# Kernel tuning notes

Measured on AMD Instinct MI355X. Metric: run time of the kernel, lower is better.

Reference implementation:

```python
import jax, jax.numpy as jnp
import numpy as np

B, D, H, W, T, C = 2, 16, 16, 16, 16, 96
NH = 4                      # num_heads
WS = (4, 4, 4, 4)           # window size
SS = (2, 2, 2, 2)           # shift size
EPS = 1e-5
HIDDEN = 4 * C


def _compute_mask():
    # Standard Swin shifted-window attention mask, extended to 4D.
    img = np.zeros((D, H, W, T), np.float32)
    sl = [[slice(0, -WS[i]), slice(-WS[i], -SS[i]), slice(-SS[i], None)] for i in range(4)]
    cnt = 0
    for a in sl[0]:
        for b in sl[1]:
            for c in sl[2]:
                for d in sl[3]:
                    img[a, b, c, d] = cnt
                    cnt += 1
    x = img.reshape(D // WS[0], WS[0], H // WS[1], WS[1], W // WS[2], WS[2], T // WS[3], WS[3])
    x = x.transpose(0, 2, 4, 6, 1, 3, 5, 7).reshape(-1, WS[0] * WS[1] * WS[2] * WS[3])
    diff = x[:, None, :] - x[:, :, None]
    return np.where(diff != 0, np.float32(-100.0), np.float32(0.0))


def setup_inputs() -> dict:
    key = jax.random.key(0)
    ks = jax.random.split(key, 6)
    w = lambda k, shape: jax.random.normal(k, shape, jnp.float32) * 0.02
    return {
        'x': jax.random.normal(ks[0], (B, D, H, W, T, C), jnp.float32),
        'mask_matrix': jnp.asarray(_compute_mask()),
        'norm1_g': jnp.ones((C,), jnp.float32), 'norm1_b': jnp.zeros((C,), jnp.float32),
        'qkv_w': w(ks[1], (3 * C, C)), 'qkv_b': jnp.zeros((3 * C,), jnp.float32),
        'proj_w': w(ks[2], (C, C)), 'proj_b': jnp.zeros((C,), jnp.float32),
        'norm2_g': jnp.ones((C,), jnp.float32), 'norm2_b': jnp.zeros((C,), jnp.float32),
        'fc1_w': w(ks[3], (HIDDEN, C)), 'fc1_b': jnp.zeros((HIDDEN,), jnp.float32),
        'fc2_w': w(ks[4], (C, HIDDEN)), 'fc2_b': jnp.zeros((C,), jnp.float32),
    }


def _ln(x, g, b):
    mu = jnp.mean(x, -1, keepdims=True)
    var = jnp.var(x, -1, keepdims=True)
    return (x - mu) * jax.lax.rsqrt(var + EPS) * g + b


def _partition(x):
    # (B, D, H, W, T, C) -> (B*nw, N, C)
    b, c = x.shape[0], x.shape[-1]
    x = x.reshape(b, D // WS[0], WS[0], H // WS[1], WS[1], W // WS[2], WS[2], T // WS[3], WS[3], c)
    x = x.transpose(0, 1, 3, 5, 7, 2, 4, 6, 8, 9)
    return x.reshape(-1, WS[0] * WS[1] * WS[2] * WS[3], c)


def _reverse(win, b):
    c = win.shape[-1]
    x = win.reshape(b, D // WS[0], H // WS[1], W // WS[2], T // WS[3], WS[0], WS[1], WS[2], WS[3], c)
    x = x.transpose(0, 1, 5, 2, 6, 3, 7, 4, 8, 9)
    return x.reshape(b, D, H, W, T, c)


def reference(x, mask_matrix, norm1_g, norm1_b, qkv_w, qkv_b, proj_w, proj_b,
              norm2_g, norm2_b, fc1_w, fc1_b, fc2_w, fc2_b):
    b, c = x.shape[0], x.shape[-1]
    hd = c // NH
    scale = hd ** -0.5
    shortcut = x
    # norm -> (no pad needed: dims divisible by window) -> cyclic shift
    xn = _ln(x, norm1_g, norm1_b)
    xs = jnp.roll(xn, shift=(-SS[0], -SS[1], -SS[2], -SS[3]), axis=(1, 2, 3, 4))
    win = _partition(xs)                              # (B_, N, C)
    B_, N, _ = win.shape
    qkv = (win @ qkv_w.T + qkv_b).reshape(B_, N, 3, NH, hd).transpose(2, 0, 3, 1, 4)
    q, k, v = qkv[0] * scale, qkv[1], qkv[2]          # (B_, NH, N, hd)
    attn = jnp.einsum('bhid,bhjd->bhij', q, k)        # (B_, NH, N, N)
    nw = mask_matrix.shape[0]
    attn = attn.reshape(B_ // nw, nw, NH, N, N) + mask_matrix[None, :, None]
    attn = jax.nn.softmax(attn.reshape(B_, NH, N, N), axis=-1)
    out = jnp.einsum('bhij,bhjd->bhid', attn, v)
    out = out.transpose(0, 2, 1, 3).reshape(B_, N, c)
    out = out @ proj_w.T + proj_b
    xr = _reverse(out, b)
    xr = jnp.roll(xr, shift=SS, axis=(1, 2, 3, 4))    # reverse cyclic shift
    x = shortcut + xr
    # MLP block
    h = _ln(x, norm2_g, norm2_b)
    h = jax.nn.gelu(h @ fc1_w.T + fc1_b, approximate=False)
    return x + (h @ fc2_w.T + fc2_b)
```

## Files before the change

### kernel.cpp

```cpp
#include <hip/hip_runtime.h>

#define TOK   131072
#define BWIN  512

typedef __attribute__((ext_vector_type(8))) short bf16x8;
typedef __attribute__((ext_vector_type(4))) float f32x4;

__device__ __forceinline__ unsigned short f2us(float f) {
  union { float f; unsigned int i; } x; x.f = f;
  return (unsigned short)((x.i + 0x7fffu + ((x.i >> 16) & 1u)) >> 16);
}
__device__ __forceinline__ unsigned cvtpk(float lo, float hi) {
  unsigned r;
  asm("v_cvt_pk_bf16_f32 %0, %1, %2" : "=v"(r) : "v"(lo), "v"(hi));
  return r;
}
typedef const __attribute__((address_space(1))) unsigned int GU32;
typedef __attribute__((address_space(3))) unsigned int LU32;
__device__ __forceinline__ void gld16(const void* g, void* l) {
  __builtin_amdgcn_global_load_lds((GU32*)g, (LU32*)l, 16, 0, 0);
}

#define IW1   0
#define IW2   40960
#define IQKV  81920
#define IPROJ 116736
#define IMG_SHORTS 133120

__global__ __launch_bounds__(256) void k_prepw(
    const float* __restrict__ fc1_w, const float* __restrict__ fc2_w,
    const float* __restrict__ qkv_w, const float* __restrict__ proj_w,
    unsigned short* __restrict__ img) {
  int i = blockIdx.x * 256 + threadIdx.x;
  float v = 0.f;
  if (i < 40960) {
    int nc = i / 10240, k = i % 10240, r = k / 104, c = k % 104;
    if (k < 9984 && c < 96) v = fc1_w[(size_t)(nc * 96 + r) * 96 + c];
  } else if (i < 81920) {
    int j = i - 40960;
    int nc = j / 10240, k = j % 10240, r = k / 104, c = k % 104;
    if (k < 9984 && c < 96) v = fc2_w[(size_t)r * 384 + nc * 96 + c];
  } else if (i < 116736) {
    int j = i - 81920;
    int h = j / 8704, k = j % 8704, r = k / 104, c = k % 104;
    if (k < 8320 && r < 72 && c < 96) {
      int grp = r / 24, rr = r - grp * 24;
      v = qkv_w[(size_t)(grp * 96 + h * 24 + rr) * 96 + c];
    }
  } else {
    int j = i - 116736;
    int h = j / 4096, k = j % 4096, r = k / 40, c = k % 40;
    if (k < 3840 && c < 24) v = proj_w[(size_t)r * 96 + h * 24 + c];
  }
  img[i] = f2us(v);
}

__global__ __launch_bounds__(256) void k_ln1(const float* __restrict__ x,
                                             const float* __restrict__ g,
                                             const float* __restrict__ b,
                                             unsigned short* __restrict__ xn) {
  const int wave = threadIdx.x >> 6, lane = threadIdx.x & 63;
  const int t = blockIdx.x * 4 + wave;
  const int b_ = t >> 8, n = t & 255;
  const int batch = b_ >> 8, wi = b_ & 255;
  const int wd = (wi >> 6) & 3, wh = (wi >> 4) & 3, ww = (wi >> 2) & 3, wt = wi & 3;
  const int aa = (n >> 6) & 3, bb = (n >> 4) & 3, cc = (n >> 2) & 3, dd = n & 3;
  const int sd = (wd * 4 + aa + 2) & 15, sh = (wh * 4 + bb + 2) & 15;
  const int sw = (ww * 4 + cc + 2) & 15, st = (wt * 4 + dd + 2) & 15;
  const size_t gg = ((((size_t)(batch * 16 + sd) * 16 + sh) * 16 + sw) * 16 + st);

  float2 f;
  if (lane < 48) f = *(const float2*)(x + gg * 96 + 2 * lane);
  else { f.x = 0.f; f.y = 0.f; }
  float s = f.x + f.y, q2 = f.x * f.x + f.y * f.y;
  #pragma unroll
  for (int m = 1; m < 64; m <<= 1) { s += __shfl_xor(s, m, 64); q2 += __shfl_xor(q2, m, 64); }
  const float mu = s * (1.f / 96.f);
  const float var = q2 * (1.f / 96.f) - mu * mu;
  const float rs = rsqrtf(fmaxf(var, 0.f) + 1e-5f);
  if (lane < 48) {
    float a0 = (f.x - mu) * rs * g[2 * lane]     + b[2 * lane];
    float a1 = (f.y - mu) * rs * g[2 * lane + 1] + b[2 * lane + 1];
    ((unsigned int*)xn)[(size_t)t * 48 + lane] = cvtpk(a0, a1);
  }
}

#define O_K   10240
#define O_VT  20480
#define O_U   28928
#define O_LB  37632
#define LDS_BYTES 75520

__global__ __launch_bounds__(256, 2) void k_win(
    const unsigned short* __restrict__ xn, const float* __restrict__ x,
    const unsigned short* __restrict__ img,
    const float* __restrict__ qkv_b, const float* __restrict__ proj_b,
    float* __restrict__ out) {
  extern __shared__ short lds[];
  short* s_q  = lds;
  short* s_k  = lds + O_K;
  short* s_vt = lds + O_VT;
  short* s_u  = lds + O_U;
  unsigned char* s_lb = (unsigned char*)(lds + O_LB);

  const int tid = threadIdx.x;
  const int w = tid >> 6, l = tid & 63, quad = l >> 4, l15 = l & 15;
  const int q0 = w * 64;
  const int b_ = blockIdx.x;
  const int batch = b_ >> 8, wi = b_ & 255;
  const int wd = (wi >> 6) & 3, wh = (wi >> 4) & 3, ww = (wi >> 2) & 3, wt = wi & 3;
  const float scale = 0.20412414523193154f;
  const f32x4 fz = {0.f, 0.f, 0.f, 0.f};

  {
    const int n = tid;
    const int aa = (n >> 6) & 3, bb = (n >> 4) & 3, cc = (n >> 2) & 3, dd = n & 3;
    const int p0 = wd * 4 + aa, p1 = wh * 4 + bb, p2 = ww * 4 + cc, p3 = wt * 4 + dd;
    const int r0 = p0 >= 14 ? 2 : (p0 >= 12 ? 1 : 0);
    const int r1 = p1 >= 14 ? 2 : (p1 >= 12 ? 1 : 0);
    const int r2 = p2 >= 14 ? 2 : (p2 >= 12 ? 1 : 0);
    const int r3 = p3 >= 14 ? 2 : (p3 >= 12 ? 1 : 0);
    s_lb[n] = (unsigned char)(((r0 * 3 + r1) * 3 + r2) * 3 + r3);
    unsigned int* qp = (unsigned int*)(s_q + n * 40 + 24);
    unsigned int* kp = (unsigned int*)(s_k + n * 40 + 24);
    #pragma unroll
    for (int i = 0; i < 8; i++) { qp[i] = 0u; kp[i] = 0u; }
    unsigned int* vz = (unsigned int*)(s_vt + 24 * 264);
    for (int i = tid; i < 8 * 132; i += 256)
      vz[i] = (i < 132) ? 0x3f803f80u : 0u;
  }
  __syncthreads();

  unsigned lj4[16];
  #pragma unroll
  for (int km = 0; km < 16; km++)
    lj4[km] = *(const unsigned*)&s_lb[km * 16 + quad * 4];

  f32x4 pacc[4][6];
  #pragma unroll
  for (int mt = 0; mt < 4; mt++)
    #pragma unroll
    for (int nt = 0; nt < 6; nt++) pacc[mt][nt] = fz;

  const unsigned short* xw = xn + (size_t)b_ * 256 * 96;

  for (int h = 0; h < 4; h++) {
    __syncthreads();
    {
      const char* gq = (const char*)(img + IQKV) + h * 17408;
      for (int j = w; j < 17; j += 4)
        gld16(gq + j * 1024 + l * 16, (char*)s_u + j * 1024);
    }
    __syncthreads();
    f32x4 acc[5][4];
    #pragma unroll
    for (int mt = 0; mt < 5; mt++)
      #pragma unroll
      for (int nt = 0; nt < 4; nt++) acc[mt][nt] = fz;
    #pragma unroll
    for (int ks = 0; ks < 3; ks++) {
      bf16x8 aw[5];
      #pragma unroll
      for (int mt = 0; mt < 5; mt++)
        aw[mt] = *(const bf16x8*)&s_u[(mt * 16 + l15) * 104 + ks * 32 + quad * 8];
      #pragma unroll
      for (int nt = 0; nt < 4; nt++) {
        bf16x8 bx = *(const bf16x8*)(xw + (size_t)(q0 + nt * 16 + l15) * 96 + ks * 32 + quad * 8);
        #pragma unroll
        for (int mt = 0; mt < 5; mt++)
          acc[mt][nt] = __builtin_amdgcn_mfma_f32_16x16x32_bf16(aw[mt], bx, acc[mt][nt], 0, 0, 0);
      }
    }
    #pragma unroll
    for (int mt = 0; mt < 5; mt++) {
      const int e0 = mt * 16 + quad * 4;
      #pragma unroll
      for (int nt = 0; nt < 4; nt++) {
        const int tok = q0 + nt * 16 + l15;
        if (e0 < 24) {
          uint2 pk;
          pk.x = cvtpk((acc[mt][nt][0] + qkv_b[h * 24 + e0]) * scale,
                       (acc[mt][nt][1] + qkv_b[h * 24 + e0 + 1]) * scale);
          pk.y = cvtpk((acc[mt][nt][2] + qkv_b[h * 24 + e0 + 2]) * scale,
                       (acc[mt][nt][3] + qkv_b[h * 24 + e0 + 3]) * scale);
          *(uint2*)&s_q[tok * 40 + e0] = pk;
        } else if (e0 < 48) {
          const int e = e0 - 24;
          uint2 pk;
          pk.x = cvtpk(acc[mt][nt][0] + qkv_b[96 + h * 24 + e],
                       acc[mt][nt][1] + qkv_b[96 + h * 24 + e + 1]);
          pk.y = cvtpk(acc[mt][nt][2] + qkv_b[96 + h * 24 + e + 2],
                       acc[mt][nt][3] + qkv_b[96 + h * 24 + e + 3]);
          *(uint2*)&s_k[tok * 40 + e] = pk;
        } else if (e0 < 72) {
          const int e = e0 - 48;
          #pragma unroll
          for (int r = 0; r < 4; r++)
            s_vt[(e + r) * 264 + tok] = (short)f2us(acc[mt][nt][r] + qkv_b[192 + h * 24 + e + r]);
        }
      }
    }
    __syncthreads();
    short* s_p = s_u + w * 2176;
    #pragma unroll 1
    for (int mt4 = 0; mt4 < 4; mt4++) {
      const int qt0 = q0 + mt4 * 16;
      f32x4 sc[16];
      #pragma unroll
      for (int km = 0; km < 16; km++) sc[km] = fz;
      bf16x8 bq = *(const bf16x8*)&s_q[(qt0 + l15) * 40 + quad * 8];
      __builtin_amdgcn_s_setprio(1);
      #pragma unroll
      for (int km = 0; km < 16; km++) {
        bf16x8 ak = *(const bf16x8*)&s_k[(km * 16 + l15) * 40 + quad * 8];
        sc[km] = __builtin_amdgcn_mfma_f32_16x16x32_bf16(ak, bq, sc[km], 0, 0, 0);
      }
      __builtin_amdgcn_s_setprio(0);
      const unsigned lq = s_lb[qt0 + l15];
      f32x4 ov[2] = {fz, fz};
      #pragma unroll
      for (int half = 0; half < 2; half++) {
        asm volatile("s_waitcnt lgkmcnt(0)" ::: "memory");
        #pragma unroll
        for (int km = half * 8; km < half * 8 + 8; km++) {
          unsigned lj = lj4[km];
          float p0 = ((lj & 255u)         == lq) ? __expf(sc[km][0]) : 0.f;
          float p1 = (((lj >> 8) & 255u)  == lq) ? __expf(sc[km][1]) : 0.f;
          float p2 = (((lj >> 16) & 255u) == lq) ? __expf(sc[km][2]) : 0.f;
          float p3 = ((lj >> 24)          == lq) ? __expf(sc[km][3]) : 0.f;
          uint2 pk;
          pk.x = cvtpk(p0, p1);
          pk.y = cvtpk(p2, p3);
          *(uint2*)&s_p[l15 * 136 + (km - half * 8) * 16 + quad * 4] = pk;
        }
        asm volatile("s_waitcnt lgkmcnt(0)" ::: "memory");
        __builtin_amdgcn_s_setprio(1);
        #pragma unroll
        for (int ks = 0; ks < 4; ks++) {
          bf16x8 bp = *(const bf16x8*)&s_p[l15 * 136 + ks * 32 + quad * 8];
          #pragma unroll
          for (int vm = 0; vm < 2; vm++) {
            bf16x8 av = *(const bf16x8*)&s_vt[(vm * 16 + l15) * 264 + half * 128 + ks * 32 + quad * 8];
            ov[vm] = __builtin_amdgcn_mfma_f32_16x16x32_bf16(av, bp, ov[vm], 0, 0, 0);
          }
        }
        __builtin_amdgcn_s_setprio(0);
      }
      float rsum = __shfl(ov[1][0], 32 + l15, 64);
      float inv = 1.f / rsum;
      uint2 o0;
      o0.x = cvtpk(ov[0][0] * inv, ov[0][1] * inv);
      o0.y = cvtpk(ov[0][2] * inv, ov[0][3] * inv);
      *(uint2*)&s_q[(qt0 + l15) * 40 + quad * 4] = o0;
      if (quad < 2) {
        uint2 o1;
        o1.x = cvtpk(ov[1][0] * inv, ov[1][1] * inv);
        o1.y = cvtpk(ov[1][2] * inv, ov[1][3] * inv);
        *(uint2*)&s_q[(qt0 + l15) * 40 + 16 + quad * 4] = o1;
      }
    }
    __syncthreads();
    {
      const char* gp = (const char*)(img + IPROJ) + h * 8192;
      for (int j = w; j < 8; j += 4)
        gld16(gp + j * 1024 + l * 16, (char*)s_u + j * 1024);
    }
    __syncthreads();
    {
      bf16x8 bp[6];
      #pragma unroll
      for (int nt = 0; nt < 6; nt++)
        bp[nt] = *(const bf16x8*)&s_u[(nt * 16 + l15) * 40 + quad * 8];
      #pragma unroll
      for (int mt = 0; mt < 4; mt++) {
        bf16x8 ao = *(const bf16x8*)&s_q[(q0 + mt * 16 + l15) * 40 + quad * 8];
        #pragma unroll
        for (int nt = 0; nt < 6; nt++)
          pacc[mt][nt] = __builtin_amdgcn_mfma_f32_16x16x32_bf16(ao, bp[nt], pacc[mt][nt], 0, 0, 0);
      }
    }
  }

  #pragma unroll
  for (int mt = 0; mt < 4; mt++) {
    #pragma unroll
    for (int r = 0; r < 4; r++) {
      int n = q0 + mt * 16 + quad * 4 + r;
      const int aa = (n >> 6) & 3, bb = (n >> 4) & 3, cc = (n >> 2) & 3, dd = n & 3;
      const int sd = (wd * 4 + aa + 2) & 15, sh = (wh * 4 + bb + 2) & 15;
      const int sw = (ww * 4 + cc + 2) & 15, st = (wt * 4 + dd + 2) & 15;
      const size_t gg = ((((size_t)(batch * 16 + sd) * 16 + sh) * 16 + sw) * 16 + st);
      #pragma unroll
      for (int nt = 0; nt < 6; nt++) {
        int c = nt * 16 + l15;
        out[gg * 96 + c] = x[gg * 96 + c] + proj_b[c] + pacc[mt][nt][r];
      }
    }
  }
}

__global__ __launch_bounds__(256, 3) void k_mlp(
    float* __restrict__ io,
    const float* __restrict__ n2g, const float* __restrict__ n2b,
    const unsigned short* __restrict__ img,
    const float* __restrict__ fc1_b, const float* __restrict__ fc2_b) {
  __shared__ __align__(16) short s_a[64 * 104];
  __shared__ __align__(16) short s_b[10240];
  __shared__ __align__(16) short s_h[64 * 104];

  const int tid = threadIdx.x;
  const int w = tid >> 6, l = tid & 63;
  const int quad = l >> 4, l15 = l & 15;
  const size_t t0 = (size_t)blockIdx.x * 64;
  const f32x4 fzero = {0.f, 0.f, 0.f, 0.f};

  for (int j = w; j < 20; j += 4)
    gld16((const char*)(img + IW1) + j * 1024 + l * 16, (char*)s_b + j * 1024);

  {
    const int r = tid >> 2, sub = tid & 3;
    const float4* base = (const float4*)(io + t0 * 96 + (size_t)tid * 24);
    float v[24];
    float s = 0.f, q = 0.f;
    #pragma unroll
    for (int j = 0; j < 6; j++) {
      float4 f = base[j];
      v[4 * j] = f.x; v[4 * j + 1] = f.y; v[4 * j + 2] = f.z; v[4 * j + 3] = f.w;
      s += f.x + f.y + f.z + f.w;
      q += f.x * f.x + f.y * f.y + f.z * f.z + f.w * f.w;
    }
    s += __shfl_xor(s, 1); q += __shfl_xor(q, 1);
    s += __shfl_xor(s, 2); q += __shfl_xor(q, 2);
    const float mu = s * (1.f / 96.f);
    const float var = q * (1.f / 96.f) - mu * mu;
    const float rs = rsqrtf(fmaxf(var, 0.f) + 1e-5f);
    unsigned int* row = (unsigned int*)&s_a[r * 104];
    #pragma unroll
    for (int jj = 0; jj < 12; jj++) {
      int k0 = sub * 24 + 2 * jj;
      float lo = (v[2 * jj]     - mu) * rs * n2g[k0]     + n2b[k0];
      float hi = (v[2 * jj + 1] - mu) * rs * n2g[k0 + 1] + n2b[k0 + 1];
      row[sub * 12 + jj] = cvtpk(lo, hi);
    }
  }

  f32x4 acc2[6];
  #pragma unroll
  for (int i = 0; i < 6; i++) acc2[i] = fzero;

  for (int nc = 0; nc < 4; nc++) {
    if (nc) {
      __syncthreads();
      for (int j = w; j < 20; j += 4)
        gld16((const char*)(img + IW1) + nc * 20480 + j * 1024 + l * 16,
              (char*)s_b + j * 1024);
    }
    __syncthreads();
    f32x4 acc1[6];
    #pragma unroll
    for (int i = 0; i < 6; i++) acc1[i] = fzero;
    #pragma unroll
    for (int ks = 0; ks < 3; ks++) {
      bf16x8 af = *(const bf16x8*)&s_a[(w * 16 + l15) * 104 + ks * 32 + quad * 8];
      #pragma unroll
      for (int nt = 0; nt < 6; nt++) {
        bf16x8 bfr = *(const bf16x8*)&s_b[(nt * 16 + l15) * 104 + ks * 32 + quad * 8];
        acc1[nt] = __builtin_amdgcn_mfma_f32_16x16x32_bf16(af, bfr, acc1[nt], 0, 0, 0);
      }
    }
    #pragma unroll
    for (int nt = 0; nt < 6; nt++) {
      int col = nt * 16 + l15;
      float bv = fc1_b[nc * 96 + col];
      #pragma unroll
      for (int r = 0; r < 4; r++) {
        float z = acc1[nt][r] + bv;
        float g = 0.5f * z * (1.f + erff(z * 0.70710678118654752f));
        s_h[(w * 16 + quad * 4 + r) * 104 + col] = (short)f2us(g);
      }
    }
    __syncthreads();
    for (int j = w; j < 20; j += 4)
      gld16((const char*)(img + IW2) + nc * 20480 + j * 1024 + l * 16,
            (char*)s_b + j * 1024);
    __syncthreads();
    #pragma unroll
    for (int ks = 0; ks < 3; ks++) {
      bf16x8 af = *(const bf16x8*)&s_h[(w * 16 + l15) * 104 + ks * 32 + quad * 8];
      #pragma unroll
      for (int nt = 0; nt < 6; nt++) {
        bf16x8 bfr = *(const bf16x8*)&s_b[(nt * 16 + l15) * 104 + ks * 32 + quad * 8];
        acc2[nt] = __builtin_amdgcn_mfma_f32_16x16x32_bf16(af, bfr, acc2[nt], 0, 0, 0);
      }
    }
  }

  #pragma unroll
  for (int nt = 0; nt < 6; nt++) {
    int col = nt * 16 + l15;
    float bv = fc2_b[col];
    #pragma unroll
    for (int r = 0; r < 4; r++) {
      size_t idx = (t0 + w * 16 + quad * 4 + r) * 96 + col;
      io[idx] = io[idx] + acc2[nt][r] + bv;
    }
  }
}

extern "C" void kernel_launch(void* const* d_in, const int* in_sizes, int n_in,
                              void* d_out, int out_size, void* d_ws, size_t ws_size,
                              hipStream_t stream) {
  const float* x      = (const float*)d_in[0];
  const float* n1g    = (const float*)d_in[2];
  const float* n1b    = (const float*)d_in[3];
  const float* qkv_w  = (const float*)d_in[4];
  const float* qkv_b  = (const float*)d_in[5];
  const float* proj_w = (const float*)d_in[6];
  const float* proj_b = (const float*)d_in[7];
  const float* n2g    = (const float*)d_in[8];
  const float* n2b    = (const float*)d_in[9];
  const float* fc1_w  = (const float*)d_in[10];
  const float* fc1_b  = (const float*)d_in[11];
  const float* fc2_w  = (const float*)d_in[12];
  const float* fc2_b  = (const float*)d_in[13];
  float* out = (float*)d_out;

  char* ws = (char*)d_ws;
  unsigned short* xn  = (unsigned short*)ws;
  unsigned short* img = (unsigned short*)(ws + 25165824u);

  (void)hipFuncSetAttribute((const void*)k_win,
                            hipFuncAttributeMaxDynamicSharedMemorySize, LDS_BYTES);
  k_prepw<<<IMG_SHORTS / 256, 256, 0, stream>>>(fc1_w, fc2_w, qkv_w, proj_w, img);
  k_ln1<<<TOK / 4, 256, 0, stream>>>(x, n1g, n1b, xn);
  k_win<<<BWIN, 256, LDS_BYTES, stream>>>(xn, x, img, qkv_b, proj_b, out);
  k_mlp<<<TOK / 64, 256, 0, stream>>>(out, n2g, n2b, img, fc1_b, fc2_b);
}
```

Before: 344.3 us.

## Pre-swizzle weights into MFMA fragment order and read them directly from global

The weight-prep kernel now writes the bf16 weights in per-lane MFMA fragment order, so each lane reads its B/A operand with one contiguous 16-byte global load. The attention and MLP kernels drop the LDS staging of weights and most of the block barriers around it. The MLP kernel also doubles its token tile to 128 rows per block (two M-tiles per wave), so each weight fragment feeds twice as many MFMAs. In exchange, weight reads go through L2/L1 instead of LDS and register pressure rises, which may lower occupancy.

```diff
diff --git a/kernel.cpp b/kernel.cpp
--- a/kernel.cpp
+++ b/kernel.cpp
@@ -15,42 +15,41 @@
   asm("v_cvt_pk_bf16_f32 %0, %1, %2" : "=v"(r) : "v"(lo), "v"(hi));
   return r;
 }
-typedef const __attribute__((address_space(1))) unsigned int GU32;
-typedef __attribute__((address_space(3))) unsigned int LU32;
-__device__ __forceinline__ void gld16(const void* g, void* l) {
-  __builtin_amdgcn_global_load_lds((GU32*)g, (LU32*)l, 16, 0, 0);
-}
 
 #define IW1   0
-#define IW2   40960
-#define IQKV  81920
-#define IPROJ 116736
-#define IMG_SHORTS 133120
+#define IW2   36864
+#define IQKV  73728
+#define IPROJ 104448
+#define IMG_SHORTS 116736
 
 __global__ __launch_bounds__(256) void k_prepw(
     const float* __restrict__ fc1_w, const float* __restrict__ fc2_w,
     const float* __restrict__ qkv_w, const float* __restrict__ proj_w,
     unsigned short* __restrict__ img) {
   int i = blockIdx.x * 256 + threadIdx.x;
+  const int l = (i >> 3) & 63, j = i & 7;
+  const int quad = l >> 4, l15 = l & 15;
   float v = 0.f;
-  if (i < 40960) {
-    int nc = i / 10240, k = i % 10240, r = k / 104, c = k % 104;
-    if (k < 9984 && c < 96) v = fc1_w[(size_t)(nc * 96 + r) * 96 + c];
-  } else if (i < 81920) {
-    int j = i - 40960;
-    int nc = j / 10240, k = j % 10240, r = k / 104, c = k % 104;
-    if (k < 9984 && c < 96) v = fc2_w[(size_t)r * 384 + nc * 96 + c];
-  } else if (i < 116736) {
-    int j = i - 81920;
-    int h = j / 8704, k = j % 8704, r = k / 104, c = k % 104;
-    if (k < 8320 && r < 72 && c < 96) {
-      int grp = r / 24, rr = r - grp * 24;
-      v = qkv_w[(size_t)(grp * 96 + h * 24 + rr) * 96 + c];
+  if (i < 36864) {
+    int f = i >> 9; int nc = f / 18, rem = f - nc * 18;
+    int ks = rem / 6, nt = rem - ks * 6;
+    v = fc1_w[(size_t)(nc * 96 + nt * 16 + l15) * 96 + ks * 32 + quad * 8 + j];
+  } else if (i < 73728) {
+    int f = (i - 36864) >> 9; int nc = f / 18, rem = f - nc * 18;
+    int ks = rem / 6, nt = rem - ks * 6;
+    v = fc2_w[(size_t)(nt * 16 + l15) * 384 + nc * 96 + ks * 32 + quad * 8 + j];
+  } else if (i < 104448) {
+    int f = (i - 73728) >> 9; int h = f / 15, rem = f - h * 15;
+    int ks = rem / 5, mt = rem - ks * 5;
+    int e = mt * 16 + l15;
+    if (e < 72) {
+      int grp = e / 24, rr = e - grp * 24;
+      v = qkv_w[(size_t)(grp * 96 + h * 24 + rr) * 96 + ks * 32 + quad * 8 + j];
     }
   } else {
-    int j = i - 116736;
-    int h = j / 4096, k = j % 4096, r = k / 40, c = k % 40;
-    if (k < 3840 && c < 24) v = proj_w[(size_t)r * 96 + h * 24 + c];
+    int f = (i - 104448) >> 9; int h = f / 6, nt = f - h * 6;
+    int e = quad * 8 + j;
+    if (e < 24) v = proj_w[(size_t)(nt * 16 + l15) * 96 + h * 24 + e];
   }
   img[i] = f2us(v);
 }
@@ -143,15 +142,10 @@
     for (int nt = 0; nt < 6; nt++) pacc[mt][nt] = fz;
 
   const unsigned short* xw = xn + (size_t)b_ * 256 * 96;
+  const unsigned short* wq = img + IQKV;
+  const unsigned short* wp = img + IPROJ;
 
   for (int h = 0; h < 4; h++) {
-    __syncthreads();
-    {
-      const char* gq = (const char*)(img + IQKV) + h * 17408;
-      for (int j = w; j < 17; j += 4)
-        gld16(gq + j * 1024 + l * 16, (char*)s_u + j * 1024);
-    }
-    __syncthreads();
     f32x4 acc[5][4];
     #pragma unroll
     for (int mt = 0; mt < 5; mt++)
@@ -162,7 +156,7 @@
       bf16x8 aw[5];
       #pragma unroll
       for (int mt = 0; mt < 5; mt++)
-        aw[mt] = *(const bf16x8*)&s_u[(mt * 16 + l15) * 104 + ks * 32 + quad * 8];
+        aw[mt] = *(const bf16x8*)(wq + ((h * 3 + ks) * 5 + mt) * 512 + l * 8);
       #pragma unroll
       for (int nt = 0; nt < 4; nt++) {
         bf16x8 bx = *(const bf16x8*)(xw + (size_t)(q0 + nt * 16 + l15) * 96 + ks * 32 + quad * 8);
@@ -259,18 +253,11 @@
         *(uint2*)&s_q[(qt0 + l15) * 40 + 16 + quad * 4] = o1;
       }
     }
-    __syncthreads();
-    {
-      const char* gp = (const char*)(img + IPROJ) + h * 8192;
-      for (int j = w; j < 8; j += 4)
-        gld16(gp + j * 1024 + l * 16, (char*)s_u + j * 1024);
-    }
-    __syncthreads();
     {
       bf16x8 bp[6];
       #pragma unroll
       for (int nt = 0; nt < 6; nt++)
-        bp[nt] = *(const bf16x8*)&s_u[(nt * 16 + l15) * 40 + quad * 8];
+        bp[nt] = *(const bf16x8*)(wp + (h * 6 + nt) * 512 + l * 8);
       #pragma unroll
       for (int mt = 0; mt < 4; mt++) {
         bf16x8 ao = *(const bf16x8*)&s_q[(q0 + mt * 16 + l15) * 40 + quad * 8];
@@ -279,6 +266,7 @@
           pacc[mt][nt] = __builtin_amdgcn_mfma_f32_16x16x32_bf16(ao, bp[nt], pacc[mt][nt], 0, 0, 0);
       }
     }
+    __syncthreads();
   }
 
   #pragma unroll
@@ -304,107 +292,108 @@
     const float* __restrict__ n2g, const float* __restrict__ n2b,
     const unsigned short* __restrict__ img,
     const float* __restrict__ fc1_b, const float* __restrict__ fc2_b) {
-  __shared__ __align__(16) short s_a[64 * 104];
-  __shared__ __align__(16) short s_b[10240];
-  __shared__ __align__(16) short s_h[64 * 104];
+  __shared__ __align__(16) short s_a[128 * 104];
+  __shared__ __align__(16) short s_h[128 * 104];
 
   const int tid = threadIdx.x;
   const int w = tid >> 6, l = tid & 63;
   const int quad = l >> 4, l15 = l & 15;
-  const size_t t0 = (size_t)blockIdx.x * 64;
-  const f32x4 fzero = {0.f, 0.f, 0.f, 0.f};
-
-  for (int j = w; j < 20; j += 4)
-    gld16((const char*)(img + IW1) + j * 1024 + l * 16, (char*)s_b + j * 1024);
+  const size_t t0 = (size_t)blockIdx.x * 128;
+  const f32x4 fz = {0.f, 0.f, 0.f, 0.f};
 
   {
-    const int r = tid >> 2, sub = tid & 3;
-    const float4* base = (const float4*)(io + t0 * 96 + (size_t)tid * 24);
-    float v[24];
+    const int r = tid >> 1, hf = tid & 1;
+    const float4* base = (const float4*)(io + (t0 + r) * 96 + hf * 48);
+    float v[48];
     float s = 0.f, q = 0.f;
     #pragma unroll
-    for (int j = 0; j < 6; j++) {
+    for (int j = 0; j < 12; j++) {
       float4 f = base[j];
       v[4 * j] = f.x; v[4 * j + 1] = f.y; v[4 * j + 2] = f.z; v[4 * j + 3] = f.w;
       s += f.x + f.y + f.z + f.w;
       q += f.x * f.x + f.y * f.y + f.z * f.z + f.w * f.w;
     }
     s += __shfl_xor(s, 1); q += __shfl_xor(q, 1);
-    s += __shfl_xor(s, 2); q += __shfl_xor(q, 2);
     const float mu = s * (1.f / 96.f);
     const float var = q * (1.f / 96.f) - mu * mu;
     const float rs = rsqrtf(fmaxf(var, 0.f) + 1e-5f);
-    unsigned int* row = (unsigned int*)&s_a[r * 104];
-    #pragma unroll
-    for (int jj = 0; jj < 12; jj++) {
-      int k0 = sub * 24 + 2 * jj;
+    unsigned int* row = (unsigned int*)&s_a[r * 104] + hf * 24;
+    #pragma unroll
+    for (int jj = 0; jj < 24; jj++) {
+      int k0 = hf * 48 + 2 * jj;
       float lo = (v[2 * jj]     - mu) * rs * n2g[k0]     + n2b[k0];
       float hi = (v[2 * jj + 1] - mu) * rs * n2g[k0 + 1] + n2b[k0 + 1];
-      row[sub * 12 + jj] = cvtpk(lo, hi);
-    }
-  }
-
-  f32x4 acc2[6];
-  #pragma unroll
-  for (int i = 0; i < 6; i++) acc2[i] = fzero;
+      row[jj] = cvtpk(lo, hi);
+    }
+  }
+
+  f32x4 acc2[2][6];
+  #pragma unroll
+  for (int m = 0; m < 2; m++)
+    #pragma unroll
+    for (int i = 0; i < 6; i++) acc2[m][i] = fz;
 
   for (int nc = 0; nc < 4; nc++) {
-    if (nc) {
-      __syncthreads();
-      for (int j = w; j < 20; j += 4)
-        gld16((const char*)(img + IW1) + nc * 20480 + j * 1024 + l * 16,
-              (char*)s_b + j * 1024);
-    }
-    __syncthreads();
-    f32x4 acc1[6];
-    #pragma unroll
-    for (int i = 0; i < 6; i++) acc1[i] = fzero;
+    f32x4 acc1[2][6];
+    #pragma unroll
+    for (int m = 0; m < 2; m++)
+      #pragma unroll
+      for (int i = 0; i < 6; i++) acc1[m][i] = fz;
     #pragma unroll
     for (int ks = 0; ks < 3; ks++) {
-      bf16x8 af = *(const bf16x8*)&s_a[(w * 16 + l15) * 104 + ks * 32 + quad * 8];
+      bf16x8 bw[6];
+      #pragma unroll
+      for (int nt = 0; nt < 6; nt++)
+        bw[nt] = *(const bf16x8*)(img + IW1 + ((nc * 3 + ks) * 6 + nt) * 512 + l * 8);
+      #pragma unroll
+      for (int m = 0; m < 2; m++) {
+        bf16x8 af = *(const bf16x8*)&s_a[(w * 32 + m * 16 + l15) * 104 + ks * 32 + quad * 8];
+        #pragma unroll
+        for (int nt = 0; nt < 6; nt++)
+          acc1[m][nt] = __builtin_amdgcn_mfma_f32_16x16x32_bf16(af, bw[nt], acc1[m][nt], 0, 0, 0);
+      }
+    }
+    #pragma unroll
+    for (int m = 0; m < 2; m++)
       #pragma unroll
       for (int nt = 0; nt < 6; nt++) {
-        bf16x8 bfr = *(const bf16x8*)&s_b[(nt * 16 + l15) * 104 + ks * 32 + quad * 8];
-        acc1[nt] = __builtin_amdgcn_mfma_f32_16x16x32_bf16(af, bfr, acc1[nt], 0, 0, 0);
-      }
-    }
+        int col = nt * 16 + l15;
+        float bv = fc1_b[nc * 96 + col];
+        #pragma unroll
+        for (int r = 0; r < 4; r++) {
+          float z = acc1[m][nt][r] + bv;
+          float g = 0.5f * z * (1.f + erff(z * 0.70710678118654752f));
+          s_h[(w * 32 + m * 16 + quad * 4 + r) * 104 + col] = (short)f2us(g);
+        }
+      }
+    #pragma unroll
+    for (int ks = 0; ks < 3; ks++) {
+      bf16x8 bw[6];
+      #pragma unroll
+      for (int nt = 0; nt < 6; nt++)
+        bw[nt] = *(const bf16x8*)(img + IW2 + ((nc * 3 + ks) * 6 + nt) * 512 + l * 8);
+      #pragma unroll
+      for (int m = 0; m < 2; m++) {
+        bf16x8 af = *(const bf16x8*)&s_h[(w * 32 + m * 16 + l15) * 104 + ks * 32 + quad * 8];
+        #pragma unroll
+        for (int nt = 0; nt < 6; nt++)
+          acc2[m][nt] = __builtin_amdgcn_mfma_f32_16x16x32_bf16(af, bw[nt], acc2[m][nt], 0, 0, 0);
+      }
+    }
+  }
+
+  #pragma unroll
+  for (int m = 0; m < 2; m++)
     #pragma unroll
     for (int nt = 0; nt < 6; nt++) {
       int col = nt * 16 + l15;
-      float bv = fc1_b[nc * 96 + col];
+      float bv = fc2_b[col];
       #pragma unroll
       for (int r = 0; r < 4; r++) {
-        float z = acc1[nt][r] + bv;
-        float g = 0.5f * z * (1.f + erff(z * 0.70710678118654752f));
-        s_h[(w * 16 + quad * 4 + r) * 104 + col] = (short)f2us(g);
-      }
-    }
-    __syncthreads();
-    for (int j = w; j < 20; j += 4)
-      gld16((const char*)(img + IW2) + nc * 20480 + j * 1024 + l * 16,
-            (char*)s_b + j * 1024);
-    __syncthreads();
-    #pragma unroll
-    for (int ks = 0; ks < 3; ks++) {
-      bf16x8 af = *(const bf16x8*)&s_h[(w * 16 + l15) * 104 + ks * 32 + quad * 8];
-      #pragma unroll
-      for (int nt = 0; nt < 6; nt++) {
-        bf16x8 bfr = *(const bf16x8*)&s_b[(nt * 16 + l15) * 104 + ks * 32 + quad * 8];
-        acc2[nt] = __builtin_amdgcn_mfma_f32_16x16x32_bf16(af, bfr, acc2[nt], 0, 0, 0);
-      }
-    }
-  }
-
-  #pragma unroll
-  for (int nt = 0; nt < 6; nt++) {
-    int col = nt * 16 + l15;
-    float bv = fc2_b[col];
-    #pragma unroll
-    for (int r = 0; r < 4; r++) {
-      size_t idx = (t0 + w * 16 + quad * 4 + r) * 96 + col;
-      io[idx] = io[idx] + acc2[nt][r] + bv;
-    }
-  }
+        size_t idx = (t0 + w * 32 + m * 16 + quad * 4 + r) * 96 + col;
+        io[idx] = io[idx] + acc2[m][nt][r] + bv;
+      }
+    }
 }
 
 extern "C" void kernel_launch(void* const* d_in, const int* in_sizes, int n_in,
@@ -434,5 +423,5 @@
   k_prepw<<<IMG_SHORTS / 256, 256, 0, stream>>>(fc1_w, fc2_w, qkv_w, proj_w, img);
   k_ln1<<<TOK / 4, 256, 0, stream>>>(x, n1g, n1b, xn);
   k_win<<<BWIN, 256, LDS_BYTES, stream>>>(xn, x, img, qkv_b, proj_b, out);
-  k_mlp<<<TOK / 64, 256, 0, stream>>>(out, n2g, n2b, img, fc1_b, fc2_b);
-}
+  k_mlp<<<TOK / 128, 256, 0, stream>>>(out, n2g, n2b, img, fc1_b, fc2_b);
+}
```

Measured after the change: 339.5 us. No clear change (-1.4%).
